# Kernel optimization log

Measured on AMD Instinct MI355X. Metric: run time of the kernel, lower is better.

## Reference

```python
import jax, jax.numpy as jnp
import numpy as np

DIM = 1024
DIM_HEAD = 64
HEADS = 16
INNER = DIM_HEAD * HEADS  # 1024
B, N1, N2 = 8, 4096, 256
EPS = 1e-5


def layer_norm(x, w, b):
    mu = jnp.mean(x, axis=-1, keepdims=True)
    var = jnp.var(x, axis=-1, keepdims=True)
    return (x - mu) * jax.lax.rsqrt(var + EPS) * w + b


def setup_inputs() -> dict:
    key = jax.random.key(0)
    ks = jax.random.split(key, 10)
    return {
        "x": jax.random.normal(ks[0], (B, N1, DIM), jnp.float32),
        "latents": jax.random.normal(ks[1], (B, N2, DIM), jnp.float32),
        "shift": jax.random.normal(ks[2], (B, DIM), jnp.float32),
        "scale": jax.random.normal(ks[3], (B, DIM), jnp.float32),
        "ln1_w": jnp.ones((DIM,), jnp.float32),
        "ln1_b": jnp.zeros((DIM,), jnp.float32),
        "ln2_w": jnp.ones((DIM,), jnp.float32),
        "ln2_b": jnp.zeros((DIM,), jnp.float32),
        "Wq": jax.random.normal(ks[4], (INNER, DIM), jnp.float32) * 0.02,
        "Wkv": jax.random.normal(ks[5], (2 * INNER, DIM), jnp.float32) * 0.02,
        "Wo": jax.random.normal(ks[6], (DIM, INNER), jnp.float32) * 0.02,
    }


def reference(x, latents, shift, scale, ln1_w, ln1_b, ln2_w, ln2_b, Wq, Wkv, Wo):
    x = layer_norm(x, ln1_w, ln1_b)                      # (b, n1, D)
    lat = layer_norm(latents, ln2_w, ln2_b)              # (b, n2, D)
    lat = lat * (1.0 + scale[:, None, :]) + shift[:, None, :]

    b, n2, _ = lat.shape
    q = jnp.einsum('bld,ed->ble', lat, Wq)               # (b, n2, inner)
    kv_in = jnp.concatenate((x, lat), axis=-2)           # (b, n1+n2, D)
    kv = jnp.einsum('bld,ed->ble', kv_in, Wkv)           # (b, n1+n2, 2*inner)
    k, v = jnp.split(kv, 2, axis=-1)

    def to_heads(t):
        bsz, L, _ = t.shape
        return t.reshape(bsz, L, HEADS, DIM_HEAD).transpose(0, 2, 1, 3)

    q, k, v = to_heads(q), to_heads(k), to_heads(v)      # (b, h, L, dh)
    attn_scale = 1.0 / np.sqrt(np.sqrt(DIM_HEAD)).astype(np.float32)
    logits = jnp.einsum('bhqd,bhkd->bhqk', q * attn_scale, k * attn_scale)
    w = jax.nn.softmax(logits.astype(jnp.float32), axis=-1).astype(logits.dtype)
    out = jnp.einsum('bhqk,bhkd->bhqd', w, v)            # (b, h, n2, dh)
    out = out.transpose(0, 2, 1, 3).reshape(b, n2, INNER)
    return jnp.einsum('ble,de->bld', out, Wo)            # (b, n2, D)
```

## Files before the change

### kernel.cpp

```cpp
#include <hip/hip_runtime.h>
#include <cstdint>
#include <cstddef>

#define B_SZ 8
#define N1 4096
#define N2 256
#define LTOT 4352
#define DIMD 1024
#define HEADS 16
#define DH 64
#define MKV (B_SZ * LTOT)
#define ATILE 64
#define AITERS (LTOT / ATILE)
#define G0B 1088

typedef _Float16 f16;
typedef f16 f16x4_t __attribute__((ext_vector_type(4)));
typedef f16 f16x8_t __attribute__((ext_vector_type(8)));
typedef float f32x4_t __attribute__((ext_vector_type(4)));

__device__ __forceinline__ void g2l16(const void* g, void* l) {
  __builtin_amdgcn_global_load_lds(
      (__attribute__((address_space(1))) void*)g,
      (__attribute__((address_space(3))) void*)l, 16, 0, 0);
}

__global__ __launch_bounds__(256) void prep_kernel(
    const float* __restrict__ x, const float* __restrict__ lat,
    const float* __restrict__ shift, const float* __restrict__ scale,
    const float* __restrict__ ln1w, const float* __restrict__ ln1b,
    const float* __restrict__ ln2w, const float* __restrict__ ln2b,
    const float* __restrict__ Wq, const float* __restrict__ Wkv,
    const float* __restrict__ Wo, f16* __restrict__ kv_in,
    f16* __restrict__ Wq16, f16* __restrict__ Wkv16, f16* __restrict__ Wo16) {
  const int bid = blockIdx.x;
  const int tid = threadIdx.x;
  if (bid >= MKV) {
    const int c = bid - MKV;
    const float* src;
    f16* dst;
    int off;
    if (c < 1024) { src = Wq; dst = Wq16; off = c; }
    else if (c < 3072) { src = Wkv; dst = Wkv16; off = c - 1024; }
    else { src = Wo; dst = Wo16; off = c - 3072; }
    const int i = off * 256 + tid;
    float4 v = ((const float4*)src)[i];
    f16x4_t o = {(f16)v.x, (f16)v.y, (f16)v.z, (f16)v.w};
    ((f16x4_t*)dst)[i] = o;
    return;
  }
  const int row = bid;
  const int b = row / LTOT;
  const int n = row - b * LTOT;
  const bool is_lat = (n >= N1);
  const float* src = is_lat ? (lat + (size_t)(b * N2 + (n - N1)) * DIMD)
                            : (x + (size_t)(b * N1 + n) * DIMD);
  float4 v = ((const float4*)src)[tid];
  float s = v.x + v.y + v.z + v.w;
  float s2 = v.x * v.x + v.y * v.y + v.z * v.z + v.w * v.w;
#pragma unroll
  for (int m = 1; m <= 32; m <<= 1) {
    s += __shfl_xor(s, m, 64);
    s2 += __shfl_xor(s2, m, 64);
  }
  __shared__ float red[8];
  const int wave = tid >> 6;
  if ((tid & 63) == 0) { red[wave * 2] = s; red[wave * 2 + 1] = s2; }
  __syncthreads();
  s = red[0] + red[2] + red[4] + red[6];
  s2 = red[1] + red[3] + red[5] + red[7];
  const float mean = s * (1.0f / DIMD);
  const float var = fmaxf(s2 * (1.0f / DIMD) - mean * mean, 0.0f);
  const float rstd = rsqrtf(var + 1e-5f);
  const float4 w4 = ((const float4*)(is_lat ? ln2w : ln1w))[tid];
  const float4 b4 = ((const float4*)(is_lat ? ln2b : ln1b))[tid];
  float y0 = (v.x - mean) * rstd * w4.x + b4.x;
  float y1 = (v.y - mean) * rstd * w4.y + b4.y;
  float y2 = (v.z - mean) * rstd * w4.z + b4.z;
  float y3 = (v.w - mean) * rstd * w4.w + b4.w;
  if (is_lat) {
    float4 sc = ((const float4*)(scale + (size_t)b * DIMD))[tid];
    float4 sh = ((const float4*)(shift + (size_t)b * DIMD))[tid];
    y0 = y0 * (1.0f + sc.x) + sh.x;
    y1 = y1 * (1.0f + sc.y) + sh.y;
    y2 = y2 * (1.0f + sc.z) + sh.z;
    y3 = y3 * (1.0f + sc.w) + sh.w;
  }
  f16x4_t o = {(f16)y0, (f16)y1, (f16)y2, (f16)y3};
  *(f16x4_t*)(kv_in + (size_t)row * DIMD + tid * 4) = o;
}

#define DS_A(buf, mh)                                                          \
  _Pragma("unroll") for (int i_ = 0; i_ < 4; i_++)                             \
  _Pragma("unroll") for (int ks_ = 0; ks_ < 2; ks_++)                          \
      aF[i_][ks_] = *(const f16x8_t*)&As[buf][mh][                             \
          (wrow * 64 + i_ * 16 + r16) * 64 + (((ks_ * 4 + g8i) ^ xk) * 8)];

#define DS_B(dst, buf, nh)                                                     \
  _Pragma("unroll") for (int j_ = 0; j_ < 2; j_++)                             \
  _Pragma("unroll") for (int ks_ = 0; ks_ < 2; ks_++)                          \
      dst[j_][ks_] = *(const f16x8_t*)&Bs[buf][nh][                            \
          (wcol * 32 + j_ * 16 + r16) * 64 + (((ks_ * 4 + g8i) ^ xk) * 8)];

#define MFMA16(mh, nh, BF)                                                     \
  __builtin_amdgcn_s_setprio(1);                                               \
  _Pragma("unroll") for (int ks_ = 0; ks_ < 2; ks_++)                          \
  _Pragma("unroll") for (int i_ = 0; i_ < 4; i_++)                             \
  _Pragma("unroll") for (int j_ = 0; j_ < 2; j_++)                             \
      acc[(mh)*4 + i_][(nh)*2 + j_] = __builtin_amdgcn_mfma_f32_16x16x32_f16(  \
          aF[i_][ks_], BF[j_][ks_], acc[(mh)*4 + i_][(nh)*2 + j_], 0, 0, 0);   \
  __builtin_amdgcn_s_setprio(0);

#define BARR asm volatile("s_barrier" ::: "memory")
#define LGKM0 asm volatile("s_waitcnt lgkmcnt(0)" ::: "memory")
#define VM4 asm volatile("s_waitcnt vmcnt(4)" ::: "memory")

__global__ __launch_bounds__(512, 2) void gemm_pre(
    const f16* __restrict__ kv_in, const f16* __restrict__ Wkv16,
    const f16* __restrict__ Wq16, f16* __restrict__ kbuf,
    f16* __restrict__ vbuf, f16* __restrict__ qbuf) {
  const int id = blockIdx.x;
  const bool is_kv = (id < G0B);
  int mt = 0, nt;
  const f16 *Abase, *Bbase;
  if (is_kv) {
    const int xcd = id & 7, l = id >> 3;
    mt = xcd * 17 + (l >> 3);
    nt = l & 7;
    Abase = kv_in + (size_t)mt * 256 * DIMD;
    Bbase = Wkv16 + (size_t)nt * 256 * DIMD;
  } else {
    const int id2 = id - G0B;
    const int bq = id2 >> 2;
    nt = id2 & 3;
    Abase = kv_in + ((size_t)(bq * LTOT + N1)) * DIMD;
    Bbase = Wq16 + (size_t)nt * 256 * DIMD;
  }
  __shared__ alignas(16) f16 As[2][2][128 * 64];
  __shared__ alignas(16) f16 Bs[2][2][128 * 64];
  const int tid = threadIdx.x;
  const int wave = tid >> 6, lane = tid & 63;
  const int wrow = wave >> 2, wcol = wave & 3;
  const int r16 = lane & 15, g8i = lane >> 4, q4 = (lane >> 4) * 4;
  const int xk = r16 & 7;
  const int t8 = tid >> 3, c8 = tid & 7;
  f32x4_t acc[8][4] = {};
  f16x8_t aF[4][2], b0F[2][2], b1F[2][2];

  const int col8 = (c8 ^ (t8 & 7)) * 8;
  const f16* Asrc = Abase + (size_t)t8 * DIMD + col8;
  const f16* Bsrc = Bbase + (size_t)((t8 >> 5) * 64 + (t8 & 31)) * DIMD + col8;

  auto stageA = [&](int kt, int buf, int mh) {
#pragma unroll
    for (int j = 0; j < 2; j++)
      g2l16(Asrc + (size_t)(j * 128 + mh * 64) * DIMD + kt * 64,
            &As[buf][mh][(j * 512 + wave * 64) * 8]);
  };
  auto stageB = [&](int kt, int buf, int nh) {
#pragma unroll
    for (int j = 0; j < 2; j++)
      g2l16(Bsrc + (size_t)(j * 128 + nh * 32) * DIMD + kt * 64,
            &Bs[buf][nh][(j * 512 + wave * 64) * 8]);
  };

  stageA(0, 0, 0); stageB(0, 0, 1); stageA(0, 0, 1); stageB(0, 0, 0);
  stageA(1, 1, 0); stageB(1, 1, 1);
  VM4; BARR;

#pragma unroll 1
  for (int it = 0; it < 8; ++it) {
    const int kA = 2 * it + 1;
    const int kB = (2 * it + 2 > 15) ? 15 : 2 * it + 2;
    const int kC = (2 * it + 3 > 15) ? 15 : 2 * it + 3;
    DS_A(0, 0); DS_B(b0F, 0, 0);
    stageA(kA, 1, 1);
    BARR; MFMA16(0, 0, b0F);
    DS_B(b1F, 0, 1);
    stageB(kA, 1, 0);
    BARR; MFMA16(0, 1, b1F);
    DS_A(0, 1);
    stageA(kB, 0, 0);
    BARR; MFMA16(1, 1, b1F);
    stageB(kB, 0, 1);
    VM4;
    BARR; MFMA16(1, 0, b0F);
    DS_A(1, 0); DS_B(b0F, 1, 0);
    stageA(kB, 0, 1);
    BARR; MFMA16(0, 0, b0F);
    DS_B(b1F, 1, 1);
    stageB(kB, 0, 0);
    BARR; MFMA16(0, 1, b1F);
    DS_A(1, 1);
    stageA(kC, 1, 0);
    BARR; MFMA16(1, 1, b1F);
    stageB(kC, 1, 1);
    VM4;
    BARR; MFMA16(1, 0, b0F);
  }
  asm volatile("s_waitcnt vmcnt(0)" ::: "memory");
  BARR;

  f16* Ep = (wave < 7) ? ((f16*)As + wave * 4608) : (f16*)Bs;
  const int ln8r = lane >> 3, ln8c = lane & 7;
  const int ln16r = lane >> 4, ln16c = lane & 15;

  if (is_kv) {
    const int m0 = mt * 256;
    const int b = m0 / LTOT;
    const int n0 = m0 - b * LTOT;
    if (nt < 4) {
      const size_t hb = (size_t)(b * HEADS + nt * 4 + wcol);
#pragma unroll
      for (int p = 0; p < 2; ++p) {
        LGKM0;
#pragma unroll
        for (int aa = 0; aa < 4; ++aa)
#pragma unroll
          for (int bj = 0; bj < 4; ++bj) {
            const int dd = (bj >> 1) * 32 + (bj & 1) * 16 + r16;
#pragma unroll
            for (int r = 0; r < 4; ++r)
              Ep[(aa * 16 + q4 + r) * 72 + dd] = (f16)acc[p * 4 + aa][bj][r];
          }
        const size_t gb = (hb * LTOT + n0 + wrow * 128 + p * 64) * DH;
#pragma unroll
        for (int t = 0; t < 8; ++t) {
          f16x8_t v = *(const f16x8_t*)&Ep[(t * 8 + ln8r) * 72 + ln8c * 8];
          *(f16x8_t*)&kbuf[gb + (size_t)(t * 8 + ln8r) * DH + ln8c * 8] = v;
        }
      }
    } else {
      const size_t hb = (size_t)(b * HEADS + (nt - 4) * 4 + wcol);
#pragma unroll
      for (int p = 0; p < 2; ++p) {
        LGKM0;
#pragma unroll
        for (int bq2 = 0; bq2 < 2; ++bq2) {
          const int bj = p * 2 + bq2;
          const int dl = bq2 * 16 + r16;
#pragma unroll
          for (int ai = 0; ai < 8; ++ai) {
            const int nl = (ai >> 2) * 64 + (ai & 3) * 16 + q4;
            f16x4_t pk = {(f16)acc[ai][bj][0], (f16)acc[ai][bj][1],
                          (f16)acc[ai][bj][2], (f16)acc[ai][bj][3]};
            *(f16x4_t*)&Ep[dl * 136 + nl] = pk;
          }
        }
        const size_t nb = (size_t)n0 + wrow * 128;
#pragma unroll
        for (int t = 0; t < 8; ++t) {
          const int dr = t * 4 + ln16r;
          f16x8_t v = *(const f16x8_t*)&Ep[dr * 136 + ln16c * 8];
          *(f16x8_t*)&vbuf[(hb * DH + p * 32 + dr) * LTOT + nb + ln16c * 8] = v;
        }
      }
    }
  } else {
    const int b = (id - G0B) >> 2;
    const size_t hb = (size_t)(b * HEADS + nt * 4 + wcol);
#pragma unroll
    for (int p = 0; p < 2; ++p) {
      LGKM0;
#pragma unroll
      for (int aa = 0; aa < 4; ++aa)
#pragma unroll
        for (int bj = 0; bj < 4; ++bj) {
          const int dd = (bj >> 1) * 32 + (bj & 1) * 16 + r16;
#pragma unroll
          for (int r = 0; r < 4; ++r)
            Ep[(aa * 16 + q4 + r) * 72 + dd] = (f16)acc[p * 4 + aa][bj][r];
        }
      const size_t gb = (hb * N2 + wrow * 128 + p * 64) * DH;
#pragma unroll
      for (int t = 0; t < 8; ++t) {
        f16x8_t v = *(const f16x8_t*)&Ep[(t * 8 + ln8r) * 72 + ln8c * 8];
        *(f16x8_t*)&qbuf[gb + (size_t)(t * 8 + ln8r) * DH + ln8c * 8] = v;
      }
    }
  }
}

__global__ __launch_bounds__(256) void gemm_out(
    const f16* __restrict__ A0, const f16* __restrict__ BT,
    float* __restrict__ outp) {
  const int id = blockIdx.x;
  const int mt = id >> 4, nt = id & 15;
  const f16* Abase = A0 + (size_t)mt * 64 * DIMD;
  const f16* Bbase = BT + (size_t)nt * 64 * DIMD;
  __shared__ alignas(16) f16 As[2][64 * 32];
  __shared__ alignas(16) f16 Bs[2][64 * 32];
  const int tid = threadIdx.x;
  const int wave = tid >> 6, lane = tid & 63;
  const int wr = wave >> 1, wc = wave & 1;
  const int r16 = lane & 15, q4 = (lane >> 4) * 4;
  const int g8sw = (((lane >> 4) ^ ((r16 >> 1) & 3)) * 8);
  const int tq = tid >> 2;
  const int colx = (((tid & 3) ^ ((tq >> 1) & 3)) * 8);
  const f16* Asrc = Abase + (size_t)tq * DIMD + colx;
  const f16* Bsrc = Bbase + (size_t)tq * DIMD + colx;
  f32x4_t acc[2][2] = {};

  auto stage = [&](int kt, int buf) {
    g2l16(Asrc + kt * 32, &As[buf][wave * 512]);
    g2l16(Bsrc + kt * 32, &Bs[buf][wave * 512]);
  };
  stage(0, 0);
#pragma unroll 1
  for (int kt = 0; kt < 32; ++kt) {
    const int cur = kt & 1;
    stage(kt + 1 < 32 ? kt + 1 : 31, cur ^ 1);
    asm volatile("s_waitcnt vmcnt(2)" ::: "memory");
    asm volatile("s_barrier" ::: "memory");
    f16x8_t a[2], bf[2];
#pragma unroll
    for (int i = 0; i < 2; i++)
      a[i] = *(const f16x8_t*)&As[cur][(wr * 32 + i * 16 + r16) * 32 + g8sw];
#pragma unroll
    for (int j = 0; j < 2; j++)
      bf[j] = *(const f16x8_t*)&Bs[cur][(wc * 32 + j * 16 + r16) * 32 + g8sw];
#pragma unroll
    for (int i = 0; i < 2; i++)
#pragma unroll
      for (int j = 0; j < 2; j++)
        acc[i][j] = __builtin_amdgcn_mfma_f32_16x16x32_f16(a[i], bf[j], acc[i][j], 0, 0, 0);
    asm volatile("s_barrier" ::: "memory");
  }
  asm volatile("s_waitcnt vmcnt(0)" ::: "memory");

  const int m0 = mt * 64, n0 = nt * 64;
#pragma unroll
  for (int i = 0; i < 2; i++) {
#pragma unroll
    for (int j = 0; j < 2; j++) {
      const int col = n0 + wc * 32 + j * 16 + r16;
#pragma unroll
      for (int r = 0; r < 4; r++)
        outp[(size_t)(m0 + wr * 32 + i * 16 + q4 + r) * DIMD + col] = acc[i][j][r];
    }
  }
}

__global__ __launch_bounds__(256, 2) void attn_kernel(
    const f16* __restrict__ qbuf, const f16* __restrict__ kbuf,
    const f16* __restrict__ vbuf, f16* __restrict__ attn_out) {
  const int bh = blockIdx.x & 127;
  const int qt = blockIdx.x >> 7;
  const int b = bh >> 4, h = bh & 15;
  const f16* qg = qbuf + ((size_t)bh * N2 + qt * 64) * DH;
  const f16* kg = kbuf + (size_t)bh * LTOT * DH;
  const f16* vg = vbuf + (size_t)bh * DH * LTOT;

  __shared__ alignas(16) f16 Ks[2][4096];
  __shared__ alignas(16) f16 Vs[2][4096];
  __shared__ alignas(16) f16 QP[4608];

  const int tid = threadIdx.x, wave = tid >> 6, lane = tid & 63;
  const int lrow = lane >> 2;
  const int r16 = lane & 15, g8 = (lane >> 4) * 8, q4 = (lane >> 4) * 4;
  const int lcol_sw = (((lane & 3) ^ ((lrow >> 1) & 3)) * 8);
  const int g8sw = (((lane >> 4) ^ ((r16 >> 1) & 3)) * 8);
  f16* Ps = &QP[wave * 1152];

#pragma unroll
  for (int i = 0; i < 2; i++) {
    const int c = wave * 2 + i, s = c >> 2, rb = (c & 3) * 16;
    g2l16(qg + (size_t)(rb + lrow) * DH + s * 32 + lcol_sw, &QP[s * 2048 + rb * 32]);
  }
  auto stage = [&](int kt, int buf) {
#pragma unroll
    for (int i = 0; i < 2; i++) {
      const int c = wave * 2 + i, s = c >> 2, rb = (c & 3) * 16;
      g2l16(kg + (size_t)(kt * ATILE + rb + lrow) * DH + s * 32 + lcol_sw,
            &Ks[buf][s * 2048 + rb * 32]);
      g2l16(vg + (size_t)(rb + lrow) * LTOT + kt * ATILE + s * 32 + lcol_sw,
            &Vs[buf][s * 2048 + rb * 32]);
    }
  };
  stage(0, 0);
  stage(1, 1);
  asm volatile("s_waitcnt vmcnt(8)" ::: "memory");
  asm volatile("s_barrier" ::: "memory");
  f16x8_t bQ[2];
#pragma unroll
  for (int s = 0; s < 2; s++)
    bQ[s] = *(const f16x8_t*)&QP[s * 2048 + (wave * 16 + r16) * 32 + g8sw];
  asm volatile("s_waitcnt lgkmcnt(0)" ::: "memory");

  f32x4_t oacc[4] = {};
  float mrow = -1e30f, lsum = 0.0f;
  const float SCL = 0.125f * 1.44269504089f;

  for (int kt = 0; kt < AITERS; kt++) {
    const int cur = kt & 1;
    asm volatile("s_waitcnt vmcnt(4)" ::: "memory");
    asm volatile("s_barrier" ::: "memory");
    f32x4_t sacc[4] = {};
    __builtin_amdgcn_s_setprio(1);
#pragma unroll
    for (int s = 0; s < 2; s++) {
      f16x8_t aK[4];
#pragma unroll
      for (int i = 0; i < 4; i++)
        aK[i] = *(const f16x8_t*)&Ks[cur][s * 2048 + (i * 16 + r16) * 32 + g8sw];
#pragma unroll
      for (int i = 0; i < 4; i++)
        sacc[i] = __builtin_amdgcn_mfma_f32_16x16x32_f16(aK[i], bQ[s], sacc[i], 0, 0, 0);
    }
    __builtin_amdgcn_s_setprio(0);
    float vmax = -1e30f;
#pragma unroll
    for (int i = 0; i < 4; i++)
#pragma unroll
      for (int r = 0; r < 4; r++) vmax = fmaxf(vmax, sacc[i][r]);
    vmax = fmaxf(vmax, __shfl_xor(vmax, 16, 64));
    vmax = fmaxf(vmax, __shfl_xor(vmax, 32, 64));
    const float pm = SCL * vmax;
    if (!__all(pm <= mrow + 8.0f)) {
      const float m_new = fmaxf(mrow, pm);
      const float alpha = exp2f(mrow - m_new);
      lsum *= alpha;
#pragma unroll
      for (int id = 0; id < 4; id++) oacc[id] *= alpha;
      mrow = m_new;
    }
    float psum = 0.0f;
#pragma unroll
    for (int i = 0; i < 4; i++) {
      f16x4_t pk;
#pragma unroll
      for (int r = 0; r < 4; r++) {
        const float p = exp2f(SCL * sacc[i][r] - mrow);
        psum += p;
        pk[r] = (f16)p;
      }
      *(f16x4_t*)&Ps[r16 * 72 + i * 16 + q4] = pk;
    }
    psum += __shfl_xor(psum, 16, 64);
    psum += __shfl_xor(psum, 32, 64);
    lsum += psum;
    __builtin_amdgcn_s_setprio(1);
#pragma unroll
    for (int s2 = 0; s2 < 2; s2++) {
      f16x8_t aV[4];
#pragma unroll
      for (int id = 0; id < 4; id++)
        aV[id] = *(const f16x8_t*)&Vs[cur][s2 * 2048 + (id * 16 + r16) * 32 + g8sw];
      const f16x8_t bP = *(const f16x8_t*)&Ps[r16 * 72 + s2 * 32 + g8];
#pragma unroll
      for (int id = 0; id < 4; id++)
        oacc[id] = __builtin_amdgcn_mfma_f32_16x16x32_f16(aV[id], bP, oacc[id], 0, 0, 0);
    }
    __builtin_amdgcn_s_setprio(0);
    asm volatile("s_waitcnt lgkmcnt(0)" ::: "memory");
    asm volatile("s_barrier" ::: "memory");
    if (kt + 2 < AITERS) stage(kt + 2, cur);
  }
  const float inv = 1.0f / lsum;
  const int q = qt * 64 + wave * 16 + r16;
  const size_t rowbase = ((size_t)(b * N2 + q)) * DIMD + h * DH;
#pragma unroll
  for (int id = 0; id < 4; id++) {
    f16x4_t pk;
#pragma unroll
    for (int r = 0; r < 4; r++) pk[r] = (f16)(oacc[id][r] * inv);
    *(f16x4_t*)&attn_out[rowbase + id * 16 + q4] = pk;
  }
}

extern "C" void kernel_launch(void* const* d_in, const int* in_sizes, int n_in,
                              void* d_out, int out_size, void* d_ws, size_t ws_size,
                              hipStream_t stream) {
  const float* x     = (const float*)d_in[0];
  const float* lat   = (const float*)d_in[1];
  const float* shift = (const float*)d_in[2];
  const float* scale = (const float*)d_in[3];
  const float* ln1w  = (const float*)d_in[4];
  const float* ln1b  = (const float*)d_in[5];
  const float* ln2w  = (const float*)d_in[6];
  const float* ln2b  = (const float*)d_in[7];
  const float* Wq    = (const float*)d_in[8];
  const float* Wkv   = (const float*)d_in[9];
  const float* Wo    = (const float*)d_in[10];
  float* outp = (float*)d_out;

  char* ws = (char*)d_ws;
  f16* kv_in = (f16*)ws;                 ws += (size_t)MKV * DIMD * 2;
  f16* Wq16  = (f16*)ws;                 ws += (size_t)1024 * 1024 * 2;
  f16* Wkv16 = (f16*)ws;                 ws += (size_t)2048 * 1024 * 2;
  f16* Wo16  = (f16*)ws;                 ws += (size_t)1024 * 1024 * 2;
  f16* qbuf  = (f16*)ws;                 ws += (size_t)B_SZ * HEADS * N2 * DH * 2;
  f16* kbuf  = (f16*)ws;                 ws += (size_t)B_SZ * HEADS * LTOT * DH * 2;
  f16* vbuf  = (f16*)ws;                 ws += (size_t)B_SZ * HEADS * LTOT * DH * 2;
  f16* aout  = (f16*)ws;                 ws += (size_t)B_SZ * N2 * DIMD * 2;

  prep_kernel<<<dim3(MKV + 4096), dim3(256), 0, stream>>>(
      x, lat, shift, scale, ln1w, ln1b, ln2w, ln2b, Wq, Wkv, Wo,
      kv_in, Wq16, Wkv16, Wo16);
  gemm_pre<<<dim3(G0B + 32), dim3(512), 0, stream>>>(
      kv_in, Wkv16, Wq16, kbuf, vbuf, qbuf);
  attn_kernel<<<dim3(512), dim3(256), 0, stream>>>(qbuf, kbuf, vbuf, aout);
  gemm_out<<<dim3(512), dim3(256), 0, stream>>>(aout, Wo16, outp);
}
```

Measured before the change: 499.7 us.

## Split attention over KV quarters with all queries per block, add merge kernel

Each attention block now processes all 256 queries of a (batch, head) pair against one quarter of the key/value sequence, instead of 64 queries against the full sequence. K/V tiles loaded into LDS are reused across four query subtiles, which cuts global K/V traffic by a factor of four. Partial outputs, row maxima and sums are written in fp32 to workspace (aliasing kv_in), and a new merge kernel combines them with log-sum-exp rescaling. The cost is an extra kernel launch, fp32 partial-output traffic, more registers for four accumulator sets, and larger LDS for Q.

```diff
diff --git a/kernel.cpp b/kernel.cpp
--- a/kernel.cpp
+++ b/kernel.cpp
@@ -11,7 +11,8 @@
 #define DH 64
 #define MKV (B_SZ * LTOT)
 #define ATILE 64
-#define AITERS (LTOT / ATILE)
+#define KVH 4
+#define AIT_H 17
 #define G0B 1088
 
 typedef _Float16 f16;
@@ -343,29 +344,28 @@
 
 __global__ __launch_bounds__(256, 2) void attn_kernel(
     const f16* __restrict__ qbuf, const f16* __restrict__ kbuf,
-    const f16* __restrict__ vbuf, f16* __restrict__ attn_out) {
+    const f16* __restrict__ vbuf, float* __restrict__ po,
+    float* __restrict__ pm, float* __restrict__ pl) {
   const int bh = blockIdx.x & 127;
-  const int qt = blockIdx.x >> 7;
-  const int b = bh >> 4, h = bh & 15;
-  const f16* qg = qbuf + ((size_t)bh * N2 + qt * 64) * DH;
-  const f16* kg = kbuf + (size_t)bh * LTOT * DH;
-  const f16* vg = vbuf + (size_t)bh * DH * LTOT;
+  const int kvh = blockIdx.x >> 7;
+  const f16* qg = qbuf + (size_t)bh * N2 * DH;
+  const f16* kg = kbuf + ((size_t)bh * LTOT + kvh * (LTOT / KVH)) * DH;
+  const f16* vg = vbuf + (size_t)bh * DH * LTOT + kvh * (LTOT / KVH);
 
   __shared__ alignas(16) f16 Ks[2][4096];
   __shared__ alignas(16) f16 Vs[2][4096];
-  __shared__ alignas(16) f16 QP[4608];
+  __shared__ alignas(16) f16 QP[18432];
 
   const int tid = threadIdx.x, wave = tid >> 6, lane = tid & 63;
   const int lrow = lane >> 2;
   const int r16 = lane & 15, g8 = (lane >> 4) * 8, q4 = (lane >> 4) * 4;
   const int lcol_sw = (((lane & 3) ^ ((lrow >> 1) & 3)) * 8);
   const int g8sw = (((lane >> 4) ^ ((r16 >> 1) & 3)) * 8);
-  f16* Ps = &QP[wave * 1152];
-
-#pragma unroll
-  for (int i = 0; i < 2; i++) {
-    const int c = wave * 2 + i, s = c >> 2, rb = (c & 3) * 16;
-    g2l16(qg + (size_t)(rb + lrow) * DH + s * 32 + lcol_sw, &QP[s * 2048 + rb * 32]);
+
+#pragma unroll
+  for (int i = 0; i < 8; i++) {
+    const int c = wave * 8 + i, s = c >> 4, rb = (c & 15) * 16;
+    g2l16(qg + (size_t)(rb + lrow) * DH + s * 32 + lcol_sw, &QP[s * 8192 + rb * 32]);
   }
   auto stage = [&](int kt, int buf) {
 #pragma unroll
@@ -381,91 +381,154 @@
   stage(1, 1);
   asm volatile("s_waitcnt vmcnt(8)" ::: "memory");
   asm volatile("s_barrier" ::: "memory");
-  f16x8_t bQ[2];
-#pragma unroll
-  for (int s = 0; s < 2; s++)
-    bQ[s] = *(const f16x8_t*)&QP[s * 2048 + (wave * 16 + r16) * 32 + g8sw];
+  f16x8_t bQ[4][2];
+#pragma unroll
+  for (int t = 0; t < 4; t++)
+#pragma unroll
+    for (int s = 0; s < 2; s++)
+      bQ[t][s] = *(const f16x8_t*)&QP[s * 8192 + (t * 64 + wave * 16 + r16) * 32 + g8sw];
   asm volatile("s_waitcnt lgkmcnt(0)" ::: "memory");
 
-  f32x4_t oacc[4] = {};
-  float mrow = -1e30f, lsum = 0.0f;
+  f32x4_t oacc[4][4] = {};
+  float mrow[4] = {-1e30f, -1e30f, -1e30f, -1e30f};
+  float lsum[4] = {0.0f, 0.0f, 0.0f, 0.0f};
   const float SCL = 0.125f * 1.44269504089f;
 
-  for (int kt = 0; kt < AITERS; kt++) {
+  for (int kt = 0; kt < AIT_H; kt++) {
     const int cur = kt & 1;
-    asm volatile("s_waitcnt vmcnt(4)" ::: "memory");
+    if (kt < AIT_H - 1) asm volatile("s_waitcnt vmcnt(4)" ::: "memory");
+    else                asm volatile("s_waitcnt vmcnt(0)" ::: "memory");
     asm volatile("s_barrier" ::: "memory");
-    f32x4_t sacc[4] = {};
-    __builtin_amdgcn_s_setprio(1);
-#pragma unroll
-    for (int s = 0; s < 2; s++) {
-      f16x8_t aK[4];
-#pragma unroll
-      for (int i = 0; i < 4; i++)
-        aK[i] = *(const f16x8_t*)&Ks[cur][s * 2048 + (i * 16 + r16) * 32 + g8sw];
-#pragma unroll
-      for (int i = 0; i < 4; i++)
-        sacc[i] = __builtin_amdgcn_mfma_f32_16x16x32_f16(aK[i], bQ[s], sacc[i], 0, 0, 0);
-    }
-    __builtin_amdgcn_s_setprio(0);
-    float vmax = -1e30f;
-#pragma unroll
-    for (int i = 0; i < 4; i++)
-#pragma unroll
-      for (int r = 0; r < 4; r++) vmax = fmaxf(vmax, sacc[i][r]);
-    vmax = fmaxf(vmax, __shfl_xor(vmax, 16, 64));
-    vmax = fmaxf(vmax, __shfl_xor(vmax, 32, 64));
-    const float pm = SCL * vmax;
-    if (!__all(pm <= mrow + 8.0f)) {
-      const float m_new = fmaxf(mrow, pm);
-      const float alpha = exp2f(mrow - m_new);
-      lsum *= alpha;
-#pragma unroll
-      for (int id = 0; id < 4; id++) oacc[id] *= alpha;
-      mrow = m_new;
-    }
-    float psum = 0.0f;
-#pragma unroll
-    for (int i = 0; i < 4; i++) {
-      f16x4_t pk;
-#pragma unroll
-      for (int r = 0; r < 4; r++) {
-        const float p = exp2f(SCL * sacc[i][r] - mrow);
-        psum += p;
-        pk[r] = (f16)p;
+    {
+      f16x8_t aK[4][2];
+#pragma unroll
+      for (int s = 0; s < 2; s++)
+#pragma unroll
+        for (int i = 0; i < 4; i++)
+          aK[i][s] = *(const f16x8_t*)&Ks[cur][s * 2048 + (i * 16 + r16) * 32 + g8sw];
+#pragma unroll
+      for (int t = 0; t < 4; t++) {
+        f32x4_t sacc[4] = {};
+        __builtin_amdgcn_s_setprio(1);
+#pragma unroll
+        for (int s = 0; s < 2; s++)
+#pragma unroll
+          for (int i = 0; i < 4; i++)
+            sacc[i] = __builtin_amdgcn_mfma_f32_16x16x32_f16(aK[i][s], bQ[t][s], sacc[i], 0, 0, 0);
+        __builtin_amdgcn_s_setprio(0);
+        float vmax = -1e30f;
+#pragma unroll
+        for (int i = 0; i < 4; i++)
+#pragma unroll
+          for (int r = 0; r < 4; r++) vmax = fmaxf(vmax, sacc[i][r]);
+        vmax = fmaxf(vmax, __shfl_xor(vmax, 16, 64));
+        vmax = fmaxf(vmax, __shfl_xor(vmax, 32, 64));
+        const float pmx = SCL * vmax;
+        if (!__all(pmx <= mrow[t] + 8.0f)) {
+          const float m_new = fmaxf(mrow[t], pmx);
+          const float alpha = exp2f(mrow[t] - m_new);
+          lsum[t] *= alpha;
+#pragma unroll
+          for (int id = 0; id < 4; id++) oacc[t][id] *= alpha;
+          mrow[t] = m_new;
+        }
+        f16* Ps = &QP[(wave * 4 + t) * 1152];
+        float psum = 0.0f;
+#pragma unroll
+        for (int i = 0; i < 4; i++) {
+          f16x4_t pk;
+#pragma unroll
+          for (int r = 0; r < 4; r++) {
+            const float p = exp2f(SCL * sacc[i][r] - mrow[t]);
+            psum += p;
+            pk[r] = (f16)p;
+          }
+          *(f16x4_t*)&Ps[r16 * 72 + i * 16 + q4] = pk;
+        }
+        psum += __shfl_xor(psum, 16, 64);
+        psum += __shfl_xor(psum, 32, 64);
+        lsum[t] += psum;
       }
-      *(f16x4_t*)&Ps[r16 * 72 + i * 16 + q4] = pk;
-    }
-    psum += __shfl_xor(psum, 16, 64);
-    psum += __shfl_xor(psum, 32, 64);
-    lsum += psum;
-    __builtin_amdgcn_s_setprio(1);
-#pragma unroll
-    for (int s2 = 0; s2 < 2; s2++) {
-      f16x8_t aV[4];
-#pragma unroll
-      for (int id = 0; id < 4; id++)
-        aV[id] = *(const f16x8_t*)&Vs[cur][s2 * 2048 + (id * 16 + r16) * 32 + g8sw];
-      const f16x8_t bP = *(const f16x8_t*)&Ps[r16 * 72 + s2 * 32 + g8];
-#pragma unroll
-      for (int id = 0; id < 4; id++)
-        oacc[id] = __builtin_amdgcn_mfma_f32_16x16x32_f16(aV[id], bP, oacc[id], 0, 0, 0);
-    }
-    __builtin_amdgcn_s_setprio(0);
+    }
+    {
+      f16x8_t aV[4][2];
+#pragma unroll
+      for (int s2 = 0; s2 < 2; s2++)
+#pragma unroll
+        for (int id = 0; id < 4; id++)
+          aV[id][s2] = *(const f16x8_t*)&Vs[cur][s2 * 2048 + (id * 16 + r16) * 32 + g8sw];
+#pragma unroll
+      for (int t = 0; t < 4; t++) {
+        const f16* Ps = &QP[(wave * 4 + t) * 1152];
+        __builtin_amdgcn_s_setprio(1);
+#pragma unroll
+        for (int s2 = 0; s2 < 2; s2++) {
+          const f16x8_t bP = *(const f16x8_t*)&Ps[r16 * 72 + s2 * 32 + g8];
+#pragma unroll
+          for (int id = 0; id < 4; id++)
+            oacc[t][id] = __builtin_amdgcn_mfma_f32_16x16x32_f16(aV[id][s2], bP, oacc[t][id], 0, 0, 0);
+        }
+        __builtin_amdgcn_s_setprio(0);
+      }
+    }
     asm volatile("s_waitcnt lgkmcnt(0)" ::: "memory");
     asm volatile("s_barrier" ::: "memory");
-    if (kt + 2 < AITERS) stage(kt + 2, cur);
-  }
-  const float inv = 1.0f / lsum;
-  const int q = qt * 64 + wave * 16 + r16;
-  const size_t rowbase = ((size_t)(b * N2 + q)) * DIMD + h * DH;
-#pragma unroll
-  for (int id = 0; id < 4; id++) {
-    f16x4_t pk;
-#pragma unroll
-    for (int r = 0; r < 4; r++) pk[r] = (f16)(oacc[id][r] * inv);
-    *(f16x4_t*)&attn_out[rowbase + id * 16 + q4] = pk;
-  }
+    if (kt + 2 < AIT_H) stage(kt + 2, cur);
+  }
+  const size_t pb = ((size_t)bh * KVH + kvh) * N2;
+#pragma unroll
+  for (int t = 0; t < 4; t++) {
+    const size_t qrow = pb + t * 64 + wave * 16 + r16;
+#pragma unroll
+    for (int id = 0; id < 4; id++)
+      *(f32x4_t*)&po[qrow * DH + id * 16 + q4] = oacc[t][id];
+    if (lane < 16) {
+      pm[pb + t * 64 + wave * 16 + lane] = mrow[t];
+      pl[pb + t * 64 + wave * 16 + lane] = lsum[t];
+    }
+  }
+}
+
+__global__ __launch_bounds__(256) void merge_kernel(
+    const float* __restrict__ po, const float* __restrict__ pm,
+    const float* __restrict__ pl, f16* __restrict__ attn_out) {
+  const int bid = blockIdx.x;
+  const int bh = bid >> 2, qc = bid & 3;
+  const int b = bh >> 4, h = bh & 15;
+  const int tid = threadIdx.x;
+  const int q = tid >> 2, dq = (tid & 3) * 16;
+  const int qg2 = qc * 64 + q;
+  const size_t r0 = (size_t)bh * KVH * N2 + qg2;
+  float mm[4], ll[4];
+#pragma unroll
+  for (int hv = 0; hv < 4; hv++) {
+    mm[hv] = pm[r0 + hv * N2];
+    ll[hv] = pl[r0 + hv * N2];
+  }
+  const float M = fmaxf(fmaxf(mm[0], mm[1]), fmaxf(mm[2], mm[3]));
+  float w[4], L = 0.0f;
+#pragma unroll
+  for (int hv = 0; hv < 4; hv++) { w[hv] = exp2f(mm[hv] - M); L += ll[hv] * w[hv]; }
+  const float inv = 1.0f / L;
+  f32x4_t acc4[4] = {};
+#pragma unroll
+  for (int hv = 0; hv < 4; hv++) {
+    const size_t rb = (r0 + hv * N2) * DH + dq;
+#pragma unroll
+    for (int j = 0; j < 4; j++) {
+      f32x4_t v = *(const f32x4_t*)&po[rb + j * 4];
+#pragma unroll
+      for (int e = 0; e < 4; e++) acc4[j][e] += v[e] * w[hv];
+    }
+  }
+  f16 outv[16];
+#pragma unroll
+  for (int j = 0; j < 4; j++)
+#pragma unroll
+    for (int e = 0; e < 4; e++) outv[j * 4 + e] = (f16)(acc4[j][e] * inv);
+  f16* dst = &attn_out[((size_t)(b * N2 + qg2)) * DIMD + h * DH + dq];
+  *(f16x8_t*)dst = *(const f16x8_t*)&outv[0];
+  *(f16x8_t*)(dst + 8) = *(const f16x8_t*)&outv[8];
 }
 
 extern "C" void kernel_launch(void* const* d_in, const int* in_sizes, int n_in,
@@ -494,11 +557,16 @@
   f16* vbuf  = (f16*)ws;                 ws += (size_t)B_SZ * HEADS * LTOT * DH * 2;
   f16* aout  = (f16*)ws;                 ws += (size_t)B_SZ * N2 * DIMD * 2;
 
+  float* po = (float*)kv_in;
+  float* pm = po + (size_t)128 * KVH * N2 * DH;
+  float* pl = pm + (size_t)128 * KVH * N2;
+
   prep_kernel<<<dim3(MKV + 4096), dim3(256), 0, stream>>>(
       x, lat, shift, scale, ln1w, ln1b, ln2w, ln2b, Wq, Wkv, Wo,
       kv_in, Wq16, Wkv16, Wo16);
   gemm_pre<<<dim3(G0B + 32), dim3(512), 0, stream>>>(
       kv_in, Wkv16, Wq16, kbuf, vbuf, qbuf);
-  attn_kernel<<<dim3(512), dim3(256), 0, stream>>>(qbuf, kbuf, vbuf, aout);
+  attn_kernel<<<dim3(512), dim3(256), 0, stream>>>(qbuf, kbuf, vbuf, po, pm, pl);
+  merge_kernel<<<dim3(512), dim3(256), 0, stream>>>(po, pm, pl, aout);
   gemm_out<<<dim3(512), dim3(256), 0, stream>>>(aout, Wo16, outp);
 }
```

Result: no change. 505.8 us (+1.2%).

## Replace 256x256 8-wave QKV GEMM with simpler 128x128 4-wave double-buffered tiles

Applied to the files above, without the earlier changes.

Rewrites the QKV projection GEMM from 256x256 output tiles with 512 threads and a hand-interleaved quarter-tile pipeline to 128x128 tiles with 256 threads and a plain two-stage double buffer. The grid grows to 4352 KV blocks plus 128 Q blocks, with new XCD-aware tile mapping and a simpler single-pass epilogue that writes K, V (transposed) and Q. The aim is better occupancy and load balance with a simpler schedule. The cost is more global and LDS traffic per FLOP from the smaller tiles, and less overlap between loads and MFMA.

```diff
diff --git a/kernel.cpp b/kernel.cpp
--- a/kernel.cpp
+++ b/kernel.cpp
@@ -12,7 +12,7 @@
 #define MKV (B_SZ * LTOT)
 #define ATILE 64
 #define AITERS (LTOT / ATILE)
-#define G0B 1088
+#define G0B 4352
 
 typedef _Float16 f16;
 typedef f16 f16x4_t __attribute__((ext_vector_type(4)));
@@ -90,193 +90,156 @@
   *(f16x4_t*)(kv_in + (size_t)row * DIMD + tid * 4) = o;
 }
 
-#define DS_A(buf, mh)                                                          \
-  _Pragma("unroll") for (int i_ = 0; i_ < 4; i_++)                             \
-  _Pragma("unroll") for (int ks_ = 0; ks_ < 2; ks_++)                          \
-      aF[i_][ks_] = *(const f16x8_t*)&As[buf][mh][                             \
-          (wrow * 64 + i_ * 16 + r16) * 64 + (((ks_ * 4 + g8i) ^ xk) * 8)];
-
-#define DS_B(dst, buf, nh)                                                     \
-  _Pragma("unroll") for (int j_ = 0; j_ < 2; j_++)                             \
-  _Pragma("unroll") for (int ks_ = 0; ks_ < 2; ks_++)                          \
-      dst[j_][ks_] = *(const f16x8_t*)&Bs[buf][nh][                            \
-          (wcol * 32 + j_ * 16 + r16) * 64 + (((ks_ * 4 + g8i) ^ xk) * 8)];
-
-#define MFMA16(mh, nh, BF)                                                     \
-  __builtin_amdgcn_s_setprio(1);                                               \
-  _Pragma("unroll") for (int ks_ = 0; ks_ < 2; ks_++)                          \
-  _Pragma("unroll") for (int i_ = 0; i_ < 4; i_++)                             \
-  _Pragma("unroll") for (int j_ = 0; j_ < 2; j_++)                             \
-      acc[(mh)*4 + i_][(nh)*2 + j_] = __builtin_amdgcn_mfma_f32_16x16x32_f16(  \
-          aF[i_][ks_], BF[j_][ks_], acc[(mh)*4 + i_][(nh)*2 + j_], 0, 0, 0);   \
-  __builtin_amdgcn_s_setprio(0);
-
 #define BARR asm volatile("s_barrier" ::: "memory")
 #define LGKM0 asm volatile("s_waitcnt lgkmcnt(0)" ::: "memory")
-#define VM4 asm volatile("s_waitcnt vmcnt(4)" ::: "memory")
-
-__global__ __launch_bounds__(512, 2) void gemm_pre(
+
+__global__ __launch_bounds__(256, 2) void gemm_pre(
     const f16* __restrict__ kv_in, const f16* __restrict__ Wkv16,
     const f16* __restrict__ Wq16, f16* __restrict__ kbuf,
     f16* __restrict__ vbuf, f16* __restrict__ qbuf) {
   const int id = blockIdx.x;
   const bool is_kv = (id < G0B);
-  int mt = 0, nt;
+  int mt = 0, nt, bq = 0, qm = 0;
   const f16 *Abase, *Bbase;
   if (is_kv) {
     const int xcd = id & 7, l = id >> 3;
-    mt = xcd * 17 + (l >> 3);
-    nt = l & 7;
-    Abase = kv_in + (size_t)mt * 256 * DIMD;
-    Bbase = Wkv16 + (size_t)nt * 256 * DIMD;
+    mt = xcd * 34 + (l >> 4);
+    nt = l & 15;
+    Abase = kv_in + (size_t)mt * 128 * DIMD;
+    Bbase = Wkv16 + (size_t)nt * 128 * DIMD;
   } else {
     const int id2 = id - G0B;
-    const int bq = id2 >> 2;
-    nt = id2 & 3;
-    Abase = kv_in + ((size_t)(bq * LTOT + N1)) * DIMD;
-    Bbase = Wq16 + (size_t)nt * 256 * DIMD;
-  }
-  __shared__ alignas(16) f16 As[2][2][128 * 64];
-  __shared__ alignas(16) f16 Bs[2][2][128 * 64];
+    bq = id2 >> 4;
+    qm = (id2 >> 3) & 1;
+    nt = id2 & 7;
+    Abase = kv_in + ((size_t)(bq * LTOT + N1 + qm * 128)) * DIMD;
+    Bbase = Wq16 + (size_t)nt * 128 * DIMD;
+  }
+  __shared__ alignas(16) f16 As[2][128 * 64];
+  __shared__ alignas(16) f16 Bs[2][128 * 64];
   const int tid = threadIdx.x;
   const int wave = tid >> 6, lane = tid & 63;
-  const int wrow = wave >> 2, wcol = wave & 3;
+  const int wr = wave >> 1, wc = wave & 1;
   const int r16 = lane & 15, g8i = lane >> 4, q4 = (lane >> 4) * 4;
   const int xk = r16 & 7;
-  const int t8 = tid >> 3, c8 = tid & 7;
-  f32x4_t acc[8][4] = {};
-  f16x8_t aF[4][2], b0F[2][2], b1F[2][2];
-
-  const int col8 = (c8 ^ (t8 & 7)) * 8;
-  const f16* Asrc = Abase + (size_t)t8 * DIMD + col8;
-  const f16* Bsrc = Bbase + (size_t)((t8 >> 5) * 64 + (t8 & 31)) * DIMD + col8;
-
-  auto stageA = [&](int kt, int buf, int mh) {
-#pragma unroll
-    for (int j = 0; j < 2; j++)
-      g2l16(Asrc + (size_t)(j * 128 + mh * 64) * DIMD + kt * 64,
-            &As[buf][mh][(j * 512 + wave * 64) * 8]);
+  f32x4_t acc[4][4] = {};
+
+  const int trow = tid >> 3;
+  const int colsw = ((tid & 7) ^ (trow & 7)) * 8;
+  const f16* Asrc = Abase + (size_t)trow * DIMD + colsw;
+  const f16* Bsrc = Bbase + (size_t)trow * DIMD + colsw;
+
+  auto stage = [&](int kt, int buf) {
+#pragma unroll
+    for (int c = 0; c < 4; c++)
+      g2l16(Asrc + (size_t)(c * 32) * DIMD + kt * 64, &As[buf][c * 2048 + tid * 8]);
+#pragma unroll
+    for (int c = 0; c < 4; c++)
+      g2l16(Bsrc + (size_t)(c * 32) * DIMD + kt * 64, &Bs[buf][c * 2048 + tid * 8]);
   };
-  auto stageB = [&](int kt, int buf, int nh) {
-#pragma unroll
-    for (int j = 0; j < 2; j++)
-      g2l16(Bsrc + (size_t)(j * 128 + nh * 32) * DIMD + kt * 64,
-            &Bs[buf][nh][(j * 512 + wave * 64) * 8]);
-  };
-
-  stageA(0, 0, 0); stageB(0, 0, 1); stageA(0, 0, 1); stageB(0, 0, 0);
-  stageA(1, 1, 0); stageB(1, 1, 1);
-  VM4; BARR;
-
+
+  stage(0, 0);
+  stage(1, 1);
 #pragma unroll 1
-  for (int it = 0; it < 8; ++it) {
-    const int kA = 2 * it + 1;
-    const int kB = (2 * it + 2 > 15) ? 15 : 2 * it + 2;
-    const int kC = (2 * it + 3 > 15) ? 15 : 2 * it + 3;
-    DS_A(0, 0); DS_B(b0F, 0, 0);
-    stageA(kA, 1, 1);
-    BARR; MFMA16(0, 0, b0F);
-    DS_B(b1F, 0, 1);
-    stageB(kA, 1, 0);
-    BARR; MFMA16(0, 1, b1F);
-    DS_A(0, 1);
-    stageA(kB, 0, 0);
-    BARR; MFMA16(1, 1, b1F);
-    stageB(kB, 0, 1);
-    VM4;
-    BARR; MFMA16(1, 0, b0F);
-    DS_A(1, 0); DS_B(b0F, 1, 0);
-    stageA(kB, 0, 1);
-    BARR; MFMA16(0, 0, b0F);
-    DS_B(b1F, 1, 1);
-    stageB(kB, 0, 0);
-    BARR; MFMA16(0, 1, b1F);
-    DS_A(1, 1);
-    stageA(kC, 1, 0);
-    BARR; MFMA16(1, 1, b1F);
-    stageB(kC, 1, 1);
-    VM4;
-    BARR; MFMA16(1, 0, b0F);
-  }
-  asm volatile("s_waitcnt vmcnt(0)" ::: "memory");
-  BARR;
-
-  f16* Ep = (wave < 7) ? ((f16*)As + wave * 4608) : (f16*)Bs;
+  for (int kt = 0; kt < 16; ++kt) {
+    const int cur = kt & 1;
+    if (kt < 15) asm volatile("s_waitcnt vmcnt(8)" ::: "memory");
+    else         asm volatile("s_waitcnt vmcnt(0)" ::: "memory");
+    BARR;
+    f16x8_t aF[4][2], bF[4][2];
+#pragma unroll
+    for (int i = 0; i < 4; i++)
+#pragma unroll
+      for (int ks = 0; ks < 2; ks++)
+        aF[i][ks] = *(const f16x8_t*)&As[cur][(wr * 64 + i * 16 + r16) * 64 +
+                                             (((ks * 4 + g8i) ^ xk) * 8)];
+#pragma unroll
+    for (int j = 0; j < 4; j++)
+#pragma unroll
+      for (int ks = 0; ks < 2; ks++)
+        bF[j][ks] = *(const f16x8_t*)&Bs[cur][(wc * 64 + j * 16 + r16) * 64 +
+                                             (((ks * 4 + g8i) ^ xk) * 8)];
+    __builtin_amdgcn_s_setprio(1);
+#pragma unroll
+    for (int ks = 0; ks < 2; ks++)
+#pragma unroll
+      for (int i = 0; i < 4; i++)
+#pragma unroll
+        for (int j = 0; j < 4; j++)
+          acc[i][j] = __builtin_amdgcn_mfma_f32_16x16x32_f16(
+              aF[i][ks], bF[j][ks], acc[i][j], 0, 0, 0);
+    __builtin_amdgcn_s_setprio(0);
+    BARR;
+    if (kt + 2 < 16) stage(kt + 2, cur);
+  }
+
+  f16* Ep = (wave < 3) ? ((f16*)As + wave * 4608) : (f16*)Bs;
   const int ln8r = lane >> 3, ln8c = lane & 7;
-  const int ln16r = lane >> 4, ln16c = lane & 15;
 
   if (is_kv) {
-    const int m0 = mt * 256;
+    const int m0 = mt * 128;
     const int b = m0 / LTOT;
     const int n0 = m0 - b * LTOT;
-    if (nt < 4) {
-      const size_t hb = (size_t)(b * HEADS + nt * 4 + wcol);
-#pragma unroll
-      for (int p = 0; p < 2; ++p) {
-        LGKM0;
-#pragma unroll
-        for (int aa = 0; aa < 4; ++aa)
-#pragma unroll
-          for (int bj = 0; bj < 4; ++bj) {
-            const int dd = (bj >> 1) * 32 + (bj & 1) * 16 + r16;
-#pragma unroll
-            for (int r = 0; r < 4; ++r)
-              Ep[(aa * 16 + q4 + r) * 72 + dd] = (f16)acc[p * 4 + aa][bj][r];
-          }
-        const size_t gb = (hb * LTOT + n0 + wrow * 128 + p * 64) * DH;
-#pragma unroll
-        for (int t = 0; t < 8; ++t) {
-          f16x8_t v = *(const f16x8_t*)&Ep[(t * 8 + ln8r) * 72 + ln8c * 8];
-          *(f16x8_t*)&kbuf[gb + (size_t)(t * 8 + ln8r) * DH + ln8c * 8] = v;
+    if (nt < 8) {
+      const size_t hb = (size_t)(b * HEADS + nt * 2 + wc);
+      LGKM0;
+#pragma unroll
+      for (int aa = 0; aa < 4; ++aa)
+#pragma unroll
+        for (int bj = 0; bj < 4; ++bj) {
+          const int dd = bj * 16 + r16;
+#pragma unroll
+          for (int r = 0; r < 4; ++r)
+            Ep[(aa * 16 + q4 + r) * 72 + dd] = (f16)acc[aa][bj][r];
+        }
+      const size_t gb = (hb * LTOT + n0 + wr * 64) * DH;
+      LGKM0;
+#pragma unroll
+      for (int t = 0; t < 8; ++t) {
+        f16x8_t v = *(const f16x8_t*)&Ep[(t * 8 + ln8r) * 72 + ln8c * 8];
+        *(f16x8_t*)&kbuf[gb + (size_t)(t * 8 + ln8r) * DH + ln8c * 8] = v;
+      }
+    } else {
+      const size_t hb = (size_t)(b * HEADS + (nt - 8) * 2 + wc);
+      LGKM0;
+#pragma unroll
+      for (int bj = 0; bj < 4; ++bj) {
+        const int dl = bj * 16 + r16;
+#pragma unroll
+        for (int aa = 0; aa < 4; ++aa) {
+          const int nl = aa * 16 + q4;
+          f16x4_t pk = {(f16)acc[aa][bj][0], (f16)acc[aa][bj][1],
+                        (f16)acc[aa][bj][2], (f16)acc[aa][bj][3]};
+          *(f16x4_t*)&Ep[dl * 72 + nl] = pk;
         }
       }
-    } else {
-      const size_t hb = (size_t)(b * HEADS + (nt - 4) * 4 + wcol);
-#pragma unroll
-      for (int p = 0; p < 2; ++p) {
-        LGKM0;
-#pragma unroll
-        for (int bq2 = 0; bq2 < 2; ++bq2) {
-          const int bj = p * 2 + bq2;
-          const int dl = bq2 * 16 + r16;
-#pragma unroll
-          for (int ai = 0; ai < 8; ++ai) {
-            const int nl = (ai >> 2) * 64 + (ai & 3) * 16 + q4;
-            f16x4_t pk = {(f16)acc[ai][bj][0], (f16)acc[ai][bj][1],
-                          (f16)acc[ai][bj][2], (f16)acc[ai][bj][3]};
-            *(f16x4_t*)&Ep[dl * 136 + nl] = pk;
-          }
-        }
-        const size_t nb = (size_t)n0 + wrow * 128;
-#pragma unroll
-        for (int t = 0; t < 8; ++t) {
-          const int dr = t * 4 + ln16r;
-          f16x8_t v = *(const f16x8_t*)&Ep[dr * 136 + ln16c * 8];
-          *(f16x8_t*)&vbuf[(hb * DH + p * 32 + dr) * LTOT + nb + ln16c * 8] = v;
-        }
+      const size_t nb = (size_t)n0 + wr * 64;
+      LGKM0;
+#pragma unroll
+      for (int t = 0; t < 8; ++t) {
+        const int dr = t * 8 + ln8r;
+        f16x8_t v = *(const f16x8_t*)&Ep[dr * 72 + ln8c * 8];
+        *(f16x8_t*)&vbuf[(hb * DH + dr) * LTOT + nb + ln8c * 8] = v;
       }
     }
   } else {
-    const int b = (id - G0B) >> 2;
-    const size_t hb = (size_t)(b * HEADS + nt * 4 + wcol);
-#pragma unroll
-    for (int p = 0; p < 2; ++p) {
-      LGKM0;
-#pragma unroll
-      for (int aa = 0; aa < 4; ++aa)
-#pragma unroll
-        for (int bj = 0; bj < 4; ++bj) {
-          const int dd = (bj >> 1) * 32 + (bj & 1) * 16 + r16;
-#pragma unroll
-          for (int r = 0; r < 4; ++r)
-            Ep[(aa * 16 + q4 + r) * 72 + dd] = (f16)acc[p * 4 + aa][bj][r];
-        }
-      const size_t gb = (hb * N2 + wrow * 128 + p * 64) * DH;
-#pragma unroll
-      for (int t = 0; t < 8; ++t) {
-        f16x8_t v = *(const f16x8_t*)&Ep[(t * 8 + ln8r) * 72 + ln8c * 8];
-        *(f16x8_t*)&qbuf[gb + (size_t)(t * 8 + ln8r) * DH + ln8c * 8] = v;
+    const size_t hb = (size_t)(bq * HEADS + nt * 2 + wc);
+    LGKM0;
+#pragma unroll
+    for (int aa = 0; aa < 4; ++aa)
+#pragma unroll
+      for (int bj = 0; bj < 4; ++bj) {
+        const int dd = bj * 16 + r16;
+#pragma unroll
+        for (int r = 0; r < 4; ++r)
+          Ep[(aa * 16 + q4 + r) * 72 + dd] = (f16)acc[aa][bj][r];
       }
+    const size_t gb = (hb * N2 + qm * 128 + wr * 64) * DH;
+    LGKM0;
+#pragma unroll
+    for (int t = 0; t < 8; ++t) {
+      f16x8_t v = *(const f16x8_t*)&Ep[(t * 8 + ln8r) * 72 + ln8c * 8];
+      *(f16x8_t*)&qbuf[gb + (size_t)(t * 8 + ln8r) * DH + ln8c * 8] = v;
     }
   }
 }
@@ -497,7 +460,7 @@
   prep_kernel<<<dim3(MKV + 4096), dim3(256), 0, stream>>>(
       x, lat, shift, scale, ln1w, ln1b, ln2w, ln2b, Wq, Wkv, Wo,
       kv_in, Wq16, Wkv16, Wo16);
-  gemm_pre<<<dim3(G0B + 32), dim3(512), 0, stream>>>(
+  gemm_pre<<<dim3(G0B + 128), dim3(256), 0, stream>>>(
       kv_in, Wkv16, Wq16, kbuf, vbuf, qbuf);
   attn_kernel<<<dim3(512), dim3(256), 0, stream>>>(qbuf, kbuf, vbuf, aout);
   gemm_out<<<dim3(512), dim3(256), 0, stream>>>(aout, Wo16, outp);
```

Result: no change. 508.8 us (+1.8%).
